# Performance work log

Measured on AMD Instinct MI355X. Metric: run time of the kernel, lower is better.

The kernel has to match this reference:

```python
import jax, jax.numpy as jnp
import numpy as np

HIDDEN = 2048
HEADS = 16
HEAD_DIM = HIDDEN // HEADS
TOP_K = 256
B, N = 1, 2048


def setup_inputs() -> dict:
    key = jax.random.key(0)
    ks = jax.random.split(key, 9)
    s = 0.02
    return {
        "hidden_states": jax.random.normal(ks[0], (B, N, HIDDEN), jnp.float32),
        "Wq": jax.random.normal(ks[1], (HIDDEN, HIDDEN), jnp.float32) * s,
        "bq": jnp.zeros((HIDDEN,), jnp.float32),
        "Wk": jax.random.normal(ks[2], (HIDDEN, HIDDEN), jnp.float32) * s,
        "bk": jnp.zeros((HIDDEN,), jnp.float32),
        "Wv": jax.random.normal(ks[3], (HIDDEN, HIDDEN), jnp.float32) * s,
        "bv": jnp.zeros((HIDDEN,), jnp.float32),
        "Wo": jax.random.normal(ks[4], (HIDDEN, HIDDEN), jnp.float32) * s,
        "bo": jnp.zeros((HIDDEN,), jnp.float32),
    }


def _split_heads(x):
    b, n, _ = x.shape
    return x.reshape(b, n, HEADS, HEAD_DIM).transpose(0, 2, 1, 3)  # b h n d


def reference(hidden_states, Wq, bq, Wk, bk, Wv, bv, Wo, bo):
    scale = 1.0 / jnp.sqrt(jnp.float32(HEAD_DIM))
    q = _split_heads(hidden_states @ Wq + bq)  # [b,h,n,d]
    k = _split_heads(hidden_states @ Wk + bk)
    v = _split_heads(hidden_states @ Wv + bv)

    # Sparse path (kv_seq_length > attention_window): dense QK^T used only to rank keys.
    scores = jnp.einsum("bhnd,bhmd->bhnm", q, k) * scale  # [b,h,n,n]
    importance = scores.mean(axis=2)  # [b,h,n] aggregate over queries
    _, idx = jax.lax.top_k(importance, TOP_K)  # [b,h,k]

    # gather selected K/V (torch.gather along seq dim)
    k_sel = jnp.take_along_axis(k, idx[..., None], axis=2)  # [b,h,k,d]
    v_sel = jnp.take_along_axis(v, idx[..., None], axis=2)

    w = jax.nn.softmax(jnp.einsum("bhnd,bhkd->bhnk", q, k_sel) * scale, axis=-1)
    out = jnp.einsum("bhnk,bhkd->bhnd", w, v_sel)  # [b,h,n,d]
    out = out.transpose(0, 2, 1, 3).reshape(hidden_states.shape[0], -1, HIDDEN)
    return out @ Wo + bo
```

## Files before the change

kernel.cpp:

```cpp
#include <hip/hip_runtime.h>


typedef __attribute__((ext_vector_type(8))) short bf16x8;
typedef __attribute__((ext_vector_type(8))) unsigned short u16x8;
typedef __attribute__((ext_vector_type(4))) float f32x4;

__device__ __forceinline__ unsigned short f2bf(float x) {
    unsigned u = __float_as_uint(x);
    u += 0x7fffu + ((u >> 16) & 1u);
    return (unsigned short)(u >> 16);
}

__device__ __forceinline__ void load_lds16(const unsigned short* g, unsigned short* l) {
    __builtin_amdgcn_global_load_lds(
        (const __attribute__((address_space(1))) unsigned int*)g,
        (__attribute__((address_space(3))) unsigned int*)l,
        16, 0, 0);
}

struct Ptr4  { const float* p[4]; };

__global__ __launch_bounds__(256) void gemm_qkv(
    const unsigned short* __restrict__ HSb,
    const unsigned short* __restrict__ WT4,
    const float* __restrict__ bq,
    const float* __restrict__ bk,
    const float* __restrict__ bv,
    const int* __restrict__ idx,
    unsigned short* __restrict__ Qb,
    unsigned short* __restrict__ Ksel,
    unsigned short* __restrict__ VselT)
{
    __shared__ __align__(16) unsigned short As[4][128][32];
    __shared__ __align__(16) unsigned short Bs[4][64][32];

    const int tid  = threadIdx.x;
    const int lane = tid & 63;
    const int wave = tid >> 6;
    const int wm = wave >> 1, wn = wave & 1;
    const int lr = lane >> 2;
    const int lc = (lane & 3) * 8;

    const int bid = blockIdx.x;

    int kv, h = 0, bm, bn;
    const unsigned short* Bt;
    long ar0, ar1;
    if (bid < 128) {
        kv = 1 + (bid >> 6);
        const int t = bid & 63;
        h  = t >> 2;
        bm = ((t >> 1) & 1) * 128;
        bn = h * 128 + (t & 1) * 64;
        Bt = WT4 + (long)kv * 4194304;
        ar0 = idx[h * 256 + bm + wave * 16 + lr];
        ar1 = idx[h * 256 + bm + wave * 16 + 64 + lr];
    } else {
        kv = 0;
        const int t = bid - 128;
        const int st = t >> 5, u = t & 31;
        bm = ((st >> 2) * 4 + (u >> 3)) * 128;
        bn = ((st & 3) * 8 + (u & 7)) * 64;
        Bt = WT4;
        ar0 = bm + wave * 16 + lr;
        ar1 = ar0 + 64;
    }

    const unsigned short* Arow0 = HSb + ar0 * 2048 + lc;
    const unsigned short* Arow1 = HSb + ar1 * 2048 + lc;
    const unsigned short* Brow0 = Bt + (long)(bn + wave * 16 + lr) * 2048 + lc;

    f32x4 acc[4][2];
#pragma unroll
    for (int i = 0; i < 4; i++)
#pragma unroll
        for (int j = 0; j < 2; j++) acc[i][j] = f32x4{0.f, 0.f, 0.f, 0.f};

    auto stage = [&](int b, int step) {
        const int k0 = step * 32;
        load_lds16(Arow0 + k0, &As[b][wave * 16][0]);
        load_lds16(Arow1 + k0, &As[b][wave * 16 + 64][0]);
        load_lds16(Brow0 + k0, &Bs[b][wave * 16][0]);
    };
    auto compute = [&](int b) {
        bf16x8 af[4], bf[2];
#pragma unroll
        for (int s = 0; s < 4; s++)
            af[s] = *(const bf16x8*)&As[b][wm * 64 + s * 16 + (lane & 15)][(lane >> 4) * 8];
#pragma unroll
        for (int t = 0; t < 2; t++)
            bf[t] = *(const bf16x8*)&Bs[b][wn * 32 + t * 16 + (lane & 15)][(lane >> 4) * 8];
#pragma unroll
        for (int s = 0; s < 4; s++)
#pragma unroll
            for (int t = 0; t < 2; t++)
                acc[s][t] = __builtin_amdgcn_mfma_f32_16x16x32_bf16(af[s], bf[t], acc[s][t], 0, 0, 0);
    };

    stage(0, 0);
    stage(1, 1);
    stage(2, 2);
#pragma unroll 4
    for (int t = 0; t < 61; ++t) {
        asm volatile("s_waitcnt vmcnt(6)" ::: "memory");
        __builtin_amdgcn_s_barrier();
        __builtin_amdgcn_sched_barrier(0);
        stage((t + 3) & 3, t + 3);
        __builtin_amdgcn_sched_barrier(0);
        compute(t & 3);
    }
    asm volatile("s_waitcnt vmcnt(6)" ::: "memory");
    __builtin_amdgcn_s_barrier();
    __builtin_amdgcn_sched_barrier(0);
    compute(1);
    asm volatile("s_waitcnt vmcnt(3)" ::: "memory");
    __builtin_amdgcn_s_barrier();
    __builtin_amdgcn_sched_barrier(0);
    compute(2);
    asm volatile("s_waitcnt vmcnt(0)" ::: "memory");
    __builtin_amdgcn_s_barrier();
    __builtin_amdgcn_sched_barrier(0);
    compute(3);

    if (kv == 0) {
#pragma unroll
        for (int s = 0; s < 4; s++) {
#pragma unroll
            for (int t = 0; t < 2; t++) {
                const int col  = bn + wn * 32 + t * 16 + (lane & 15);
                const int row0 = bm + wm * 64 + s * 16 + (lane >> 4) * 4;
                const float bb = bq[col];
#pragma unroll
                for (int r = 0; r < 4; r++)
                    Qb[(long)(row0 + r) * 2048 + col] = f2bf(acc[s][t][r] + bb);
            }
        }
    } else {
        const float* bp = (kv == 1) ? bk : bv;
#pragma unroll
        for (int s = 0; s < 4; s++) {
#pragma unroll
            for (int t = 0; t < 2; t++) {
                const int col = bn + wn * 32 + t * 16 + (lane & 15);
                const int dd  = col & 127;
                const float bb = bp[col];
                const int j0 = bm + wm * 64 + s * 16 + (lane >> 4) * 4;
#pragma unroll
                for (int r = 0; r < 4; r++) {
                    const int j = j0 + r;
                    const unsigned short h16 = f2bf(acc[s][t][r] + bb);
                    if (kv == 1) Ksel [h * 32768 + j * 128 + dd] = h16;
                    else         VselT[h * 32768 + dd * 256 + j] = h16;
                }
            }
        }
    }
}

__global__ __launch_bounds__(256) void gemm_o(
    const unsigned short* __restrict__ Att,
    const unsigned short* __restrict__ WoT,
    const float* __restrict__ bo,
    float* __restrict__ out)
{
    __shared__ __align__(16) unsigned short As[4][128][32];
    __shared__ __align__(16) unsigned short Bs[4][64][32];

    const int tid  = threadIdx.x;
    const int lane = tid & 63;
    const int wave = tid >> 6;
    const int wm = wave >> 1, wn = wave & 1;
    const int lr  = lane >> 2;
    const int scc = (((lane & 3) ^ ((lr >> 1) & 3))) * 8;
    const int rc  = (((lane >> 4) ^ (((lane & 15) >> 1) & 3))) * 8;

    const int t0 = blockIdx.x;
    const int tl = (t0 & 7) * 64 + (t0 >> 3);
    const int st = tl >> 5, u = tl & 31;
    const int bm = ((st >> 2) * 4 + (u >> 3)) * 128;
    const int bn = ((st & 3) * 8 + (u & 7)) * 64;

    const unsigned short* Arow0 = Att + (long)(bm + wave * 16 + lr) * 2048 + scc;
    const unsigned short* Arow1 = Arow0 + 64 * 2048;
    const unsigned short* Brow0 = WoT + (long)(bn + wave * 16 + lr) * 2048 + scc;

    f32x4 acc[4][2];
#pragma unroll
    for (int i = 0; i < 4; i++)
#pragma unroll
        for (int j = 0; j < 2; j++) acc[i][j] = f32x4{0.f, 0.f, 0.f, 0.f};

    auto stage = [&](int b, int step) {
        const int k0 = step * 32;
        load_lds16(Arow0 + k0, &As[b][wave * 16][0]);
        load_lds16(Arow1 + k0, &As[b][wave * 16 + 64][0]);
        load_lds16(Brow0 + k0, &Bs[b][wave * 16][0]);
    };
    auto compute = [&](int b) {
        bf16x8 af[4], bf[2];
#pragma unroll
        for (int s = 0; s < 4; s++)
            af[s] = *(const bf16x8*)&As[b][wm * 64 + s * 16 + (lane & 15)][rc];
#pragma unroll
        for (int t = 0; t < 2; t++)
            bf[t] = *(const bf16x8*)&Bs[b][wn * 32 + t * 16 + (lane & 15)][rc];
#pragma unroll
        for (int s = 0; s < 4; s++)
#pragma unroll
            for (int t = 0; t < 2; t++)
                acc[s][t] = __builtin_amdgcn_mfma_f32_16x16x32_bf16(af[s], bf[t], acc[s][t], 0, 0, 0);
    };

    stage(0, 0);
    stage(1, 1);
    stage(2, 2);
#pragma unroll 4
    for (int t = 0; t < 61; ++t) {
        asm volatile("s_waitcnt vmcnt(6)" ::: "memory");
        __builtin_amdgcn_s_barrier();
        __builtin_amdgcn_sched_barrier(0);
        stage((t + 3) & 3, t + 3);
        __builtin_amdgcn_sched_barrier(0);
        compute(t & 3);
    }
    asm volatile("s_waitcnt vmcnt(6)" ::: "memory");
    __builtin_amdgcn_s_barrier();
    __builtin_amdgcn_sched_barrier(0);
    compute(1);
    asm volatile("s_waitcnt vmcnt(3)" ::: "memory");
    __builtin_amdgcn_s_barrier();
    __builtin_amdgcn_sched_barrier(0);
    compute(2);
    asm volatile("s_waitcnt vmcnt(0)" ::: "memory");
    __builtin_amdgcn_s_barrier();
    __builtin_amdgcn_sched_barrier(0);
    compute(3);

#pragma unroll
    for (int s = 0; s < 4; s++) {
#pragma unroll
        for (int t = 0; t < 2; t++) {
            const int col  = bn + wn * 32 + t * 16 + (lane & 15);
            const int row0 = bm + wm * 64 + s * 16 + (lane >> 4) * 4;
            const float bb = bo[col];
#pragma unroll
            for (int r = 0; r < 4; r++)
                out[(long)(row0 + r) * 2048 + col] = acc[s][t][r] + bb;
        }
    }
}

#define QS_OFF(c)  ((c) * 2048)
#define KS_OFF(c)  (4096 + (c) * 8192)
#define PS_OFF     0
#define VS_OFF(c)  (16896 + (c) * 4096)

__global__ __launch_bounds__(256, 2) void attn_kernel(
    const unsigned short* __restrict__ Qb,
    const unsigned short* __restrict__ Ksel,
    const unsigned short* __restrict__ VselT,
    unsigned short* __restrict__ Att)
{
    __shared__ __align__(16) unsigned short smem[25088];
    __shared__ float linv[64];

    const int tid  = threadIdx.x;
    const int lane = tid & 63;
    const int wave = tid >> 6;
    const int bm = blockIdx.x * 64;
    const int h  = blockIdx.y;
    const int lr  = lane >> 2;
    const int scc = (((lane & 3) ^ ((lr >> 1) & 3))) * 8;
    const int rc  = (((lane >> 4) ^ (((lane & 15) >> 1) & 3))) * 8;

    const unsigned short* Kh = Ksel  + h * 32768;
    const unsigned short* Vh = VselT + h * 32768;

    f32x4 acc[16];
#pragma unroll
    for (int t = 0; t < 16; t++) acc[t] = f32x4{0.f, 0.f, 0.f, 0.f};

#pragma unroll
    for (int c2 = 0; c2 < 2; c2++) {
        __syncthreads();
#pragma unroll
        for (int c = 0; c < 2; c++) {
            const int k0 = c2 * 64 + c * 32;
            load_lds16(Qb + (long)(bm + wave * 16 + lr) * 2048 + h * 128 + k0 + scc,
                       &smem[QS_OFF(c) + wave * 512]);
#pragma unroll
            for (int q = 0; q < 4; q++)
                load_lds16(Kh + (wave * 64 + q * 16 + lr) * 128 + k0 + scc,
                           &smem[KS_OFF(c) + (wave * 64 + q * 16) * 32]);
        }
        __syncthreads();
#pragma unroll
        for (int kk = 0; kk < 2; kk++) {
            bf16x8 af = *(const bf16x8*)&smem[QS_OFF(kk) + (wave * 16 + (lane & 15)) * 32 + rc];
#pragma unroll
            for (int t = 0; t < 16; t++) {
                bf16x8 bfv = *(const bf16x8*)&smem[KS_OFF(kk) + (t * 16 + (lane & 15)) * 32 + rc];
                acc[t] = __builtin_amdgcn_mfma_f32_16x16x32_bf16(af, bfv, acc[t], 0, 0, 0);
            }
        }
    }
    __syncthreads();

    const float se = 0.08838834764831845f * 1.4426950408889634f;
#pragma unroll
    for (int r = 0; r < 4; r++) {
        float mx = -3.0e38f;
#pragma unroll
        for (int t = 0; t < 16; t++) mx = fmaxf(mx, acc[t][r]);
#pragma unroll
        for (int off = 1; off < 16; off <<= 1) mx = fmaxf(mx, __shfl_xor(mx, off));
        float sum = 0.f;
#pragma unroll
        for (int t = 0; t < 16; t++) {
            float p = exp2f((acc[t][r] - mx) * se);
            acc[t][r] = p;
            sum += p;
        }
#pragma unroll
        for (int off = 1; off < 16; off <<= 1) sum += __shfl_xor(sum, off);
        const int row = wave * 16 + (lane >> 4) * 4 + r;
#pragma unroll
        for (int t = 0; t < 16; t++)
            smem[PS_OFF + row * 264 + t * 16 + (lane & 15)] = f2bf(acc[t][r]);
        if ((lane & 15) == 0) linv[row] = 1.0f / sum;
    }

    const int wm2 = wave >> 1, wn2 = wave & 1;
    f32x4 acc2[2][4];
#pragma unroll
    for (int i = 0; i < 2; i++)
#pragma unroll
        for (int j = 0; j < 4; j++) acc2[i][j] = f32x4{0.f, 0.f, 0.f, 0.f};

#pragma unroll
    for (int c2 = 0; c2 < 4; c2++) {
#pragma unroll
        for (int c = 0; c < 2; c++) {
            const int j0 = c2 * 64 + c * 32;
#pragma unroll
            for (int q = 0; q < 2; q++)
                load_lds16(Vh + (wave * 32 + q * 16 + lr) * 256 + j0 + scc,
                           &smem[VS_OFF(c) + (wave * 32 + q * 16) * 32]);
        }
        __syncthreads();
#pragma unroll
        for (int c = 0; c < 2; c++) {
            const int j0 = c2 * 64 + c * 32;
            bf16x8 af2[2], bf2v[4];
#pragma unroll
            for (int s2 = 0; s2 < 2; s2++)
                af2[s2] = *(const bf16x8*)&smem[PS_OFF + (wm2 * 32 + s2 * 16 + (lane & 15)) * 264 + j0 + (lane >> 4) * 8];
#pragma unroll
            for (int t2 = 0; t2 < 4; t2++)
                bf2v[t2] = *(const bf16x8*)&smem[VS_OFF(c) + (wn2 * 64 + t2 * 16 + (lane & 15)) * 32 + rc];
#pragma unroll
            for (int s2 = 0; s2 < 2; s2++)
#pragma unroll
                for (int t2 = 0; t2 < 4; t2++)
                    acc2[s2][t2] = __builtin_amdgcn_mfma_f32_16x16x32_bf16(af2[s2], bf2v[t2], acc2[s2][t2], 0, 0, 0);
        }
        __syncthreads();
    }

#pragma unroll
    for (int s2 = 0; s2 < 2; s2++) {
#pragma unroll
        for (int t2 = 0; t2 < 4; t2++) {
            const int d = wn2 * 64 + t2 * 16 + (lane & 15);
#pragma unroll
            for (int r = 0; r < 4; r++) {
                const int row = wm2 * 32 + s2 * 16 + (lane >> 4) * 4 + r;
                float v = acc2[s2][t2][r] * linv[row];
                Att[(long)(bm + row) * 2048 + h * 128 + d] = f2bf(v);
            }
        }
    }
}

__global__ __launch_bounds__(256) void prep_kernel(Ptr4 srcs, unsigned short* __restrict__ WT4,
                                                   const float* __restrict__ hs,
                                                   double* __restrict__ part) {
    const int b = blockIdx.x;
    const int tid = threadIdx.x;
    if (b < 4096) {
        __shared__ float tile[64][65];
        const int z = b >> 10, xy = b & 1023;
        const float* W = srcs.p[z];
        unsigned short* WT = WT4 + (long)z * 4194304;
        const int bx = (xy & 31) * 64;
        const int by = (xy >> 5) * 64;
        const int x = tid & 63, y = tid >> 6;
#pragma unroll
        for (int i = 0; i < 64; i += 4)
            tile[y + i][x] = W[(long)(by + y + i) * 2048 + bx + x];
        __syncthreads();
#pragma unroll
        for (int i = 0; i < 64; i += 4)
            WT[(long)(bx + y + i) * 2048 + by + x] = f2bf(tile[x][y + i]);
    } else {
        const int c = b - 4096;
        const int col = (c & 7) * 256 + tid;
        const int r0  = (c >> 3) * 32;
        double a = 0.0;
#pragma unroll 4
        for (int r = 0; r < 32; r++) a += (double)hs[(long)(r0 + r) * 2048 + col];
        part[(long)(c >> 3) * 2048 + col] = a;
    }
}

__global__ void fill_kernel(float* p, float v, long n) {
    long i = ((long)blockIdx.x * blockDim.x + threadIdx.x) * 4;
    if (i + 3 < n) { p[i] = v; p[i+1] = v; p[i+2] = v; p[i+3] = v; }
}

__global__ __launch_bounds__(256) void mean_qsum_part(const double* __restrict__ part,
                                                      const float* __restrict__ Wq,
                                                      double* __restrict__ partq) {
    __shared__ float hsb[32];
    const int j  = blockIdx.x * 256 + threadIdx.x;
    const int i0 = blockIdx.y * 32;
    if (threadIdx.x < 32) {
        double s = 0.0;
#pragma unroll 4
        for (int g = 0; g < 64; g++) s += part[(long)g * 2048 + i0 + threadIdx.x];
        hsb[threadIdx.x] = (float)(s * (1.0 / 2048.0));
    }
    __syncthreads();
    double a = 0.0;
#pragma unroll 4
    for (int r = 0; r < 32; r++)
        a += (double)hsb[r] * (double)Wq[(long)(i0 + r) * 2048 + j];
    partq[(long)blockIdx.y * 2048 + j] = a;
}

__global__ void qsum_fin(const double* __restrict__ partq, const float* __restrict__ bq,
                         float* __restrict__ qbar) {
    const int j = blockIdx.x * 64 + threadIdx.x;
    double s = (double)bq[j];
#pragma unroll 4
    for (int g = 0; g < 64; g++) s += partq[(long)g * 2048 + j];
    qbar[j] = (float)s;
}

__global__ __launch_bounds__(256) void u_kernel(const float* __restrict__ Wk,
                                                const float* __restrict__ qbar,
                                                float* __restrict__ U) {
    const int i = blockIdx.x, t = threadIdx.x;
#pragma unroll
    for (int r = 0; r < 2; r++) {
        const int e = r * 1024 + t * 4;
        float4 w = *(const float4*)(Wk + (long)i * 2048 + e);
        float4 q = *(const float4*)(qbar + e);
        float a = w.x * q.x + w.y * q.y + w.z * q.z + w.w * q.w;
#pragma unroll
        for (int off = 16; off; off >>= 1) a += __shfl_xor(a, off);
        if ((t & 31) == 0) U[(long)i * 16 + r * 8 + (t >> 5)] = a;
    }
}

__global__ __launch_bounds__(256) void cast_imp_kernel(const float* __restrict__ hs,
                                                       const float* __restrict__ U,
                                                       unsigned short* __restrict__ HSb,
                                                       float* __restrict__ imp) {
    __shared__ float red[4][4][16];
    const int m0 = blockIdx.x * 4, t = threadIdx.x;

    float va[4][8];
#pragma unroll
    for (int r = 0; r < 4; r++) {
        const float4 v0 = *(const float4*)(hs + (long)(m0 + r) * 2048 + t * 8);
        const float4 v1 = *(const float4*)(hs + (long)(m0 + r) * 2048 + t * 8 + 4);
        va[r][0] = v0.x; va[r][1] = v0.y; va[r][2] = v0.z; va[r][3] = v0.w;
        va[r][4] = v1.x; va[r][5] = v1.y; va[r][6] = v1.z; va[r][7] = v1.w;
        u16x8 hb;
#pragma unroll
        for (int j = 0; j < 8; j++) hb[j] = f2bf(va[r][j]);
        *(u16x8*)(HSb + (long)(m0 + r) * 2048 + t * 8) = hb;
    }

    float p[4][16];
#pragma unroll
    for (int r = 0; r < 4; r++)
#pragma unroll
        for (int h = 0; h < 16; h++) p[r][h] = 0.f;

    const float4* Uq = (const float4*)(U + (long)t * 128);
#pragma unroll
    for (int j = 0; j < 8; j++) {
        const float4 u0 = Uq[j * 4 + 0];
        const float4 u1 = Uq[j * 4 + 1];
        const float4 u2 = Uq[j * 4 + 2];
        const float4 u3 = Uq[j * 4 + 3];
#pragma unroll
        for (int r = 0; r < 4; r++) {
            const float v = va[r][j];
            p[r][0]  += v * u0.x; p[r][1]  += v * u0.y; p[r][2]  += v * u0.z; p[r][3]  += v * u0.w;
            p[r][4]  += v * u1.x; p[r][5]  += v * u1.y; p[r][6]  += v * u1.z; p[r][7]  += v * u1.w;
            p[r][8]  += v * u2.x; p[r][9]  += v * u2.y; p[r][10] += v * u2.z; p[r][11] += v * u2.w;
            p[r][12] += v * u3.x; p[r][13] += v * u3.y; p[r][14] += v * u3.z; p[r][15] += v * u3.w;
        }
    }

#pragma unroll
    for (int off = 32; off; off >>= 1)
#pragma unroll
        for (int r = 0; r < 4; r++)
#pragma unroll
            for (int h = 0; h < 16; h++) p[r][h] += __shfl_down(p[r][h], off);
    if ((t & 63) == 0)
#pragma unroll
        for (int r = 0; r < 4; r++)
#pragma unroll
            for (int h = 0; h < 16; h++) red[t >> 6][r][h] = p[r][h];
    __syncthreads();
    if (t < 64) {
        const int h = t & 15, r = t >> 4;
        imp[(long)h * 2048 + m0 + r] =
            red[0][r][h] + red[1][r][h] + red[2][r][h] + red[3][r][h];
    }
}

__global__ __launch_bounds__(64) void topk_idx(const float* __restrict__ imp,
                                               int* __restrict__ idx) {
    const int h = blockIdx.x;
    const int lane = threadIdx.x;
    unsigned u[32];
#pragma unroll
    for (int r = 0; r < 32; r++) {
        unsigned x = __float_as_uint(imp[(long)h * 2048 + r * 64 + lane]);
        u[r] = (x & 0x80000000u) ? ~x : (x | 0x80000000u);
    }
    unsigned cur = 0;
    for (int b = 31; b >= 0; b--) {
        const unsigned cand = cur | (1u << b);
        int tot = 0;
#pragma unroll
        for (int r = 0; r < 32; r++)
            tot += (int)__popcll(__ballot(u[r] >= cand));
        if (tot >= 256) cur = cand;
    }
    const unsigned long long below = (1ull << lane) - 1ull;
    int pos[32];
    int base = 0;
#pragma unroll
    for (int r = 0; r < 32; r++) {
        const bool q = u[r] > cur;
        const unsigned long long m = __ballot(q);
        pos[r] = q ? base + (int)__popcll(m & below) : -1;
        base += (int)__popcll(m);
    }
#pragma unroll
    for (int r = 0; r < 32; r++) {
        const bool q = (u[r] == cur);
        const unsigned long long m = __ballot(q);
        if (q) {
            const int p = base + (int)__popcll(m & below);
            pos[r] = (p < 256) ? p : -1;
        }
        base += (int)__popcll(m);
    }
#pragma unroll
    for (int r = 0; r < 32; r++)
        if (pos[r] >= 0) idx[h * 256 + pos[r]] = r * 64 + lane;
}

extern "C" void kernel_launch(void* const* d_in, const int* in_sizes, int n_in,
                              void* d_out, int out_size, void* d_ws, size_t ws_size,
                              hipStream_t stream)
{
    const float* hs = (const float*)d_in[0];
    const float* Wq = (const float*)d_in[1];
    const float* bq = (const float*)d_in[2];
    const float* Wk = (const float*)d_in[3];
    const float* bk = (const float*)d_in[4];
    const float* Wv = (const float*)d_in[5];
    const float* bv = (const float*)d_in[6];
    const float* Wo = (const float*)d_in[7];
    const float* bo = (const float*)d_in[8];

    char* ws = (char*)d_ws;
    size_t off = 0;
    auto alloc = [&](size_t b) -> void* {
        void* p = ws + off;
        off = (off + b + 255) & ~(size_t)255;
        return p;
    };
    unsigned short* HSb   = (unsigned short*)alloc(8388608);
    unsigned short* WT4   = (unsigned short*)alloc(4 * 8388608);
    unsigned short* Qb    = (unsigned short*)alloc(8388608);
    unsigned short* Att   = (unsigned short*)alloc(8388608);
    unsigned short* Ksel  = (unsigned short*)alloc(1048576);
    unsigned short* VselT = (unsigned short*)alloc(1048576);
    double* part  = (double*)alloc(1048576);
    double* partq = (double*)alloc(1048576);
    float* qbar  = (float*)alloc(8192);
    float* U     = (float*)alloc(131072);
    float* imp   = (float*)alloc(131072);
    int*   idx   = (int*)alloc(16384);

    if (off > ws_size) {
        fill_kernel<<<4096, 256, 0, stream>>>((float*)d_out, 12345.0f, (long)out_size);
        return;
    }

    unsigned short* WoT = WT4 + 3 * 4194304;

    prep_kernel<<<4608, 256, 0, stream>>>(Ptr4{{Wq, Wk, Wv, Wo}}, WT4, hs, part);

    mean_qsum_part<<<dim3(8, 64), 256, 0, stream>>>(part, Wq, partq);
    qsum_fin<<<32, 64, 0, stream>>>(partq, bq, qbar);
    u_kernel<<<2048, 256, 0, stream>>>(Wk, qbar, U);
    cast_imp_kernel<<<512, 256, 0, stream>>>(hs, U, HSb, imp);

    topk_idx<<<16, 64, 0, stream>>>(imp, idx);

    gemm_qkv<<<640, 256, 0, stream>>>(HSb, WT4, bq, bk, bv, idx, Qb, Ksel, VselT);

    attn_kernel<<<dim3(32, 16), 256, 0, stream>>>(Qb, Ksel, VselT, Att);

    gemm_o<<<512, 256, 0, stream>>>(Att, WoT, bo, (float*)d_out);
}
```

Baseline: 278.1 us.

## Fuse Q projection into attention kernel and split off K/V selection GEMM

The Q projection is moved out of the combined QKV GEMM and into the attention kernel. Each attention block now computes its 64x128 Q tile from hidden states and Wq straight into LDS, which removes the Qb round trip through global memory. The QKV launch shrinks to a 128-block K/V-only kernel, so the attention launch is now serialized behind a smaller GEMM. In exchange, attention LDS use grows, which may reduce occupancy, and the per-block Q GEMM uses a smaller tile with less reuse of hidden-state rows than the previous 128x64 tiling.

```diff
diff --git a/kernel.cpp b/kernel.cpp
--- a/kernel.cpp
+++ b/kernel.cpp
@@ -20,14 +20,12 @@
 
 struct Ptr4  { const float* p[4]; };
 
-__global__ __launch_bounds__(256) void gemm_qkv(
+__global__ __launch_bounds__(256) void gemm_kv(
     const unsigned short* __restrict__ HSb,
     const unsigned short* __restrict__ WT4,
-    const float* __restrict__ bq,
     const float* __restrict__ bk,
     const float* __restrict__ bv,
     const int* __restrict__ idx,
-    unsigned short* __restrict__ Qb,
     unsigned short* __restrict__ Ksel,
     unsigned short* __restrict__ VselT)
 {
@@ -42,29 +40,14 @@
     const int lc = (lane & 3) * 8;
 
     const int bid = blockIdx.x;
-
-    int kv, h = 0, bm, bn;
-    const unsigned short* Bt;
-    long ar0, ar1;
-    if (bid < 128) {
-        kv = 1 + (bid >> 6);
-        const int t = bid & 63;
-        h  = t >> 2;
-        bm = ((t >> 1) & 1) * 128;
-        bn = h * 128 + (t & 1) * 64;
-        Bt = WT4 + (long)kv * 4194304;
-        ar0 = idx[h * 256 + bm + wave * 16 + lr];
-        ar1 = idx[h * 256 + bm + wave * 16 + 64 + lr];
-    } else {
-        kv = 0;
-        const int t = bid - 128;
-        const int st = t >> 5, u = t & 31;
-        bm = ((st >> 2) * 4 + (u >> 3)) * 128;
-        bn = ((st & 3) * 8 + (u & 7)) * 64;
-        Bt = WT4;
-        ar0 = bm + wave * 16 + lr;
-        ar1 = ar0 + 64;
-    }
+    const int kv = 1 + (bid >> 6);
+    const int t = bid & 63;
+    const int h  = t >> 2;
+    const int bm = ((t >> 1) & 1) * 128;
+    const int bn = h * 128 + (t & 1) * 64;
+    const unsigned short* Bt = WT4 + (long)kv * 4194304;
+    const long ar0 = idx[h * 256 + bm + wave * 16 + lr];
+    const long ar1 = idx[h * 256 + bm + wave * 16 + 64 + lr];
 
     const unsigned short* Arow0 = HSb + ar0 * 2048 + lc;
     const unsigned short* Arow1 = HSb + ar1 * 2048 + lc;
@@ -88,26 +71,26 @@
         for (int s = 0; s < 4; s++)
             af[s] = *(const bf16x8*)&As[b][wm * 64 + s * 16 + (lane & 15)][(lane >> 4) * 8];
 #pragma unroll
-        for (int t = 0; t < 2; t++)
-            bf[t] = *(const bf16x8*)&Bs[b][wn * 32 + t * 16 + (lane & 15)][(lane >> 4) * 8];
+        for (int t2 = 0; t2 < 2; t2++)
+            bf[t2] = *(const bf16x8*)&Bs[b][wn * 32 + t2 * 16 + (lane & 15)][(lane >> 4) * 8];
 #pragma unroll
         for (int s = 0; s < 4; s++)
 #pragma unroll
-            for (int t = 0; t < 2; t++)
-                acc[s][t] = __builtin_amdgcn_mfma_f32_16x16x32_bf16(af[s], bf[t], acc[s][t], 0, 0, 0);
+            for (int t2 = 0; t2 < 2; t2++)
+                acc[s][t2] = __builtin_amdgcn_mfma_f32_16x16x32_bf16(af[s], bf[t2], acc[s][t2], 0, 0, 0);
     };
 
     stage(0, 0);
     stage(1, 1);
     stage(2, 2);
 #pragma unroll 4
-    for (int t = 0; t < 61; ++t) {
+    for (int t2 = 0; t2 < 61; ++t2) {
         asm volatile("s_waitcnt vmcnt(6)" ::: "memory");
         __builtin_amdgcn_s_barrier();
         __builtin_amdgcn_sched_barrier(0);
-        stage((t + 3) & 3, t + 3);
+        stage((t2 + 3) & 3, t2 + 3);
         __builtin_amdgcn_sched_barrier(0);
-        compute(t & 3);
+        compute(t2 & 3);
     }
     asm volatile("s_waitcnt vmcnt(6)" ::: "memory");
     __builtin_amdgcn_s_barrier();
@@ -122,36 +105,21 @@
     __builtin_amdgcn_sched_barrier(0);
     compute(3);
 
-    if (kv == 0) {
-#pragma unroll
-        for (int s = 0; s < 4; s++) {
-#pragma unroll
-            for (int t = 0; t < 2; t++) {
-                const int col  = bn + wn * 32 + t * 16 + (lane & 15);
-                const int row0 = bm + wm * 64 + s * 16 + (lane >> 4) * 4;
-                const float bb = bq[col];
-#pragma unroll
-                for (int r = 0; r < 4; r++)
-                    Qb[(long)(row0 + r) * 2048 + col] = f2bf(acc[s][t][r] + bb);
-            }
-        }
-    } else {
-        const float* bp = (kv == 1) ? bk : bv;
-#pragma unroll
-        for (int s = 0; s < 4; s++) {
-#pragma unroll
-            for (int t = 0; t < 2; t++) {
-                const int col = bn + wn * 32 + t * 16 + (lane & 15);
-                const int dd  = col & 127;
-                const float bb = bp[col];
-                const int j0 = bm + wm * 64 + s * 16 + (lane >> 4) * 4;
-#pragma unroll
-                for (int r = 0; r < 4; r++) {
-                    const int j = j0 + r;
-                    const unsigned short h16 = f2bf(acc[s][t][r] + bb);
-                    if (kv == 1) Ksel [h * 32768 + j * 128 + dd] = h16;
-                    else         VselT[h * 32768 + dd * 256 + j] = h16;
-                }
+    const float* bp = (kv == 1) ? bk : bv;
+#pragma unroll
+    for (int s = 0; s < 4; s++) {
+#pragma unroll
+        for (int t2 = 0; t2 < 2; t2++) {
+            const int col = bn + wn * 32 + t2 * 16 + (lane & 15);
+            const int dd  = col & 127;
+            const float bb = bp[col];
+            const int j0 = bm + wm * 64 + s * 16 + (lane >> 4) * 4;
+#pragma unroll
+            for (int r = 0; r < 4; r++) {
+                const int j = j0 + r;
+                const unsigned short h16 = f2bf(acc[s][t2][r] + bb);
+                if (kv == 1) Ksel [h * 32768 + j * 128 + dd] = h16;
+                else         VselT[h * 32768 + dd * 256 + j] = h16;
             }
         }
     }
@@ -250,18 +218,20 @@
     }
 }
 
-#define QS_OFF(c)  ((c) * 2048)
-#define KS_OFF(c)  (4096 + (c) * 8192)
-#define PS_OFF     0
-#define VS_OFF(c)  (16896 + (c) * 4096)
-
-__global__ __launch_bounds__(256, 2) void attn_kernel(
-    const unsigned short* __restrict__ Qb,
+#define KS2_OFF(c)  ((c) * 8192)
+#define PS2_OFF     0
+#define QS2_OFF     24576
+#define VS2_OFF(c)  (24576 + (c) * 4096)
+
+__global__ __launch_bounds__(256, 2) void attn_fused(
+    const unsigned short* __restrict__ HSb,
+    const unsigned short* __restrict__ WT4,
+    const float* __restrict__ bq,
     const unsigned short* __restrict__ Ksel,
     const unsigned short* __restrict__ VselT,
     unsigned short* __restrict__ Att)
 {
-    __shared__ __align__(16) unsigned short smem[25088];
+    __shared__ __align__(16) unsigned short smem[33280];
     __shared__ float linv[64];
 
     const int tid  = threadIdx.x;
@@ -270,12 +240,88 @@
     const int bm = blockIdx.x * 64;
     const int h  = blockIdx.y;
     const int lr  = lane >> 2;
+    const int lc  = (lane & 3) * 8;
     const int scc = (((lane & 3) ^ ((lr >> 1) & 3))) * 8;
     const int rc  = (((lane >> 4) ^ (((lane & 15) >> 1) & 3))) * 8;
 
     const unsigned short* Kh = Ksel  + h * 32768;
     const unsigned short* Vh = VselT + h * 32768;
 
+    {
+        const unsigned short* Arow = HSb + (long)(bm + wave * 16 + lr) * 2048 + lc;
+        const unsigned short* Brow0 = WT4 + (long)(h * 128 + wave * 16 + lr) * 2048 + lc;
+        const unsigned short* Brow1 = Brow0 + 64 * 2048;
+
+        f32x4 acc[4][2];
+#pragma unroll
+        for (int i = 0; i < 4; i++)
+#pragma unroll
+            for (int j = 0; j < 2; j++) acc[i][j] = f32x4{0.f, 0.f, 0.f, 0.f};
+
+        auto stage = [&](int b, int step) {
+            const int k0 = step * 32;
+            load_lds16(Arow + k0, &smem[b * 2048 + wave * 16 * 32]);
+            load_lds16(Brow0 + k0, &smem[8192 + b * 4096 + wave * 16 * 32]);
+            load_lds16(Brow1 + k0, &smem[8192 + b * 4096 + (64 + wave * 16) * 32]);
+        };
+        auto compute = [&](int b) {
+            bf16x8 af[4], bf[2];
+#pragma unroll
+            for (int s = 0; s < 4; s++)
+                af[s] = *(const bf16x8*)&smem[b * 2048 + (s * 16 + (lane & 15)) * 32 + (lane >> 4) * 8];
+#pragma unroll
+            for (int t = 0; t < 2; t++)
+                bf[t] = *(const bf16x8*)&smem[8192 + b * 4096 + (wave * 32 + t * 16 + (lane & 15)) * 32 + (lane >> 4) * 8];
+#pragma unroll
+            for (int s = 0; s < 4; s++)
+#pragma unroll
+                for (int t = 0; t < 2; t++)
+                    acc[s][t] = __builtin_amdgcn_mfma_f32_16x16x32_bf16(af[s], bf[t], acc[s][t], 0, 0, 0);
+        };
+
+        stage(0, 0);
+        stage(1, 1);
+        stage(2, 2);
+#pragma unroll 4
+        for (int t = 0; t < 61; ++t) {
+            asm volatile("s_waitcnt vmcnt(6)" ::: "memory");
+            __builtin_amdgcn_s_barrier();
+            __builtin_amdgcn_sched_barrier(0);
+            stage((t + 3) & 3, t + 3);
+            __builtin_amdgcn_sched_barrier(0);
+            compute(t & 3);
+        }
+        asm volatile("s_waitcnt vmcnt(6)" ::: "memory");
+        __builtin_amdgcn_s_barrier();
+        __builtin_amdgcn_sched_barrier(0);
+        compute(1);
+        asm volatile("s_waitcnt vmcnt(3)" ::: "memory");
+        __builtin_amdgcn_s_barrier();
+        __builtin_amdgcn_sched_barrier(0);
+        compute(2);
+        asm volatile("s_waitcnt vmcnt(0)" ::: "memory");
+        __builtin_amdgcn_s_barrier();
+        __builtin_amdgcn_sched_barrier(0);
+        compute(3);
+
+        float bb[2];
+#pragma unroll
+        for (int t = 0; t < 2; t++)
+            bb[t] = bq[h * 128 + wave * 32 + t * 16 + (lane & 15)];
+#pragma unroll
+        for (int s = 0; s < 4; s++)
+#pragma unroll
+            for (int t = 0; t < 2; t++) {
+                const int col = wave * 32 + t * 16 + (lane & 15);
+#pragma unroll
+                for (int r = 0; r < 4; r++) {
+                    const int row = s * 16 + (lane >> 4) * 4 + r;
+                    smem[QS2_OFF + row * 136 + col] = f2bf(acc[s][t][r] + bb[t]);
+                }
+            }
+    }
+    __syncthreads();
+
     f32x4 acc[16];
 #pragma unroll
     for (int t = 0; t < 16; t++) acc[t] = f32x4{0.f, 0.f, 0.f, 0.f};
@@ -286,20 +332,19 @@
 #pragma unroll
         for (int c = 0; c < 2; c++) {
             const int k0 = c2 * 64 + c * 32;
-            load_lds16(Qb + (long)(bm + wave * 16 + lr) * 2048 + h * 128 + k0 + scc,
-                       &smem[QS_OFF(c) + wave * 512]);
 #pragma unroll
             for (int q = 0; q < 4; q++)
                 load_lds16(Kh + (wave * 64 + q * 16 + lr) * 128 + k0 + scc,
-                           &smem[KS_OFF(c) + (wave * 64 + q * 16) * 32]);
+                           &smem[KS2_OFF(c) + (wave * 64 + q * 16) * 32]);
         }
         __syncthreads();
 #pragma unroll
         for (int kk = 0; kk < 2; kk++) {
-            bf16x8 af = *(const bf16x8*)&smem[QS_OFF(kk) + (wave * 16 + (lane & 15)) * 32 + rc];
+            bf16x8 af = *(const bf16x8*)&smem[QS2_OFF + (wave * 16 + (lane & 15)) * 136
+                                              + c2 * 64 + kk * 32 + (lane >> 4) * 8];
 #pragma unroll
             for (int t = 0; t < 16; t++) {
-                bf16x8 bfv = *(const bf16x8*)&smem[KS_OFF(kk) + (t * 16 + (lane & 15)) * 32 + rc];
+                bf16x8 bfv = *(const bf16x8*)&smem[KS2_OFF(kk) + (t * 16 + (lane & 15)) * 32 + rc];
                 acc[t] = __builtin_amdgcn_mfma_f32_16x16x32_bf16(af, bfv, acc[t], 0, 0, 0);
             }
         }
@@ -326,7 +371,7 @@
         const int row = wave * 16 + (lane >> 4) * 4 + r;
 #pragma unroll
         for (int t = 0; t < 16; t++)
-            smem[PS_OFF + row * 264 + t * 16 + (lane & 15)] = f2bf(acc[t][r]);
+            smem[PS2_OFF + row * 264 + t * 16 + (lane & 15)] = f2bf(acc[t][r]);
         if ((lane & 15) == 0) linv[row] = 1.0f / sum;
     }
 
@@ -345,7 +390,7 @@
 #pragma unroll
             for (int q = 0; q < 2; q++)
                 load_lds16(Vh + (wave * 32 + q * 16 + lr) * 256 + j0 + scc,
-                           &smem[VS_OFF(c) + (wave * 32 + q * 16) * 32]);
+                           &smem[VS2_OFF(c) + (wave * 32 + q * 16) * 32]);
         }
         __syncthreads();
 #pragma unroll
@@ -354,10 +399,10 @@
             bf16x8 af2[2], bf2v[4];
 #pragma unroll
             for (int s2 = 0; s2 < 2; s2++)
-                af2[s2] = *(const bf16x8*)&smem[PS_OFF + (wm2 * 32 + s2 * 16 + (lane & 15)) * 264 + j0 + (lane >> 4) * 8];
+                af2[s2] = *(const bf16x8*)&smem[PS2_OFF + (wm2 * 32 + s2 * 16 + (lane & 15)) * 264 + j0 + (lane >> 4) * 8];
 #pragma unroll
             for (int t2 = 0; t2 < 4; t2++)
-                bf2v[t2] = *(const bf16x8*)&smem[VS_OFF(c) + (wn2 * 64 + t2 * 16 + (lane & 15)) * 32 + rc];
+                bf2v[t2] = *(const bf16x8*)&smem[VS2_OFF(c) + (wn2 * 64 + t2 * 16 + (lane & 15)) * 32 + rc];
 #pragma unroll
             for (int s2 = 0; s2 < 2; s2++)
 #pragma unroll
@@ -592,7 +637,6 @@
     };
     unsigned short* HSb   = (unsigned short*)alloc(8388608);
     unsigned short* WT4   = (unsigned short*)alloc(4 * 8388608);
-    unsigned short* Qb    = (unsigned short*)alloc(8388608);
     unsigned short* Att   = (unsigned short*)alloc(8388608);
     unsigned short* Ksel  = (unsigned short*)alloc(1048576);
     unsigned short* VselT = (unsigned short*)alloc(1048576);
@@ -619,9 +663,9 @@
 
     topk_idx<<<16, 64, 0, stream>>>(imp, idx);
 
-    gemm_qkv<<<640, 256, 0, stream>>>(HSb, WT4, bq, bk, bv, idx, Qb, Ksel, VselT);
-
-    attn_kernel<<<dim3(32, 16), 256, 0, stream>>>(Qb, Ksel, VselT, Att);
+    gemm_kv<<<128, 256, 0, stream>>>(HSb, WT4, bk, bv, idx, Ksel, VselT);
+
+    attn_fused<<<dim3(32, 16), 256, 0, stream>>>(HSb, WT4, bq, Ksel, VselT, Att);
 
     gemm_o<<<512, 256, 0, stream>>>(Att, WoT, bo, (float*)d_out);
 }
```

After: 293.0 us. 1.05x slower.

## Load QKV GEMM B operand directly to registers and drop block barriers

Applied to the files above, without the earlier changes.

The QKV projection GEMM now gives each wave its own 32-row A slice, staged in a private LDS region. Each wave loads the full 64-column B tile straight from global memory into registers, double-buffered. This removes shared B staging and all workgroup barriers from the main loop, since waves no longer share LDS data. The cost is that every wave re-reads the same B data from global/L2, four times the B traffic, plus more VGPR pressure from register double buffering. The vmcnt waits now have to cover both the direct loads and the LDS DMA.

```diff
diff --git a/kernel.cpp b/kernel.cpp
--- a/kernel.cpp
+++ b/kernel.cpp
@@ -31,13 +31,11 @@
     unsigned short* __restrict__ Ksel,
     unsigned short* __restrict__ VselT)
 {
-    __shared__ __align__(16) unsigned short As[4][128][32];
-    __shared__ __align__(16) unsigned short Bs[4][64][32];
+    __shared__ __align__(16) unsigned short As[4][4][32][32];
 
     const int tid  = threadIdx.x;
     const int lane = tid & 63;
     const int wave = tid >> 6;
-    const int wm = wave >> 1, wn = wave & 1;
     const int lr = lane >> 2;
     const int lc = (lane & 3) * 8;
 
@@ -53,8 +51,8 @@
         bm = ((t >> 1) & 1) * 128;
         bn = h * 128 + (t & 1) * 64;
         Bt = WT4 + (long)kv * 4194304;
-        ar0 = idx[h * 256 + bm + wave * 16 + lr];
-        ar1 = idx[h * 256 + bm + wave * 16 + 64 + lr];
+        ar0 = idx[h * 256 + bm + wave * 32 + lr];
+        ar1 = idx[h * 256 + bm + wave * 32 + 16 + lr];
     } else {
         kv = 0;
         const int t = bid - 128;
@@ -62,93 +60,107 @@
         bm = ((st >> 2) * 4 + (u >> 3)) * 128;
         bn = ((st & 3) * 8 + (u & 7)) * 64;
         Bt = WT4;
-        ar0 = bm + wave * 16 + lr;
-        ar1 = ar0 + 64;
+        ar0 = bm + wave * 32 + lr;
+        ar1 = ar0 + 16;
     }
 
     const unsigned short* Arow0 = HSb + ar0 * 2048 + lc;
     const unsigned short* Arow1 = HSb + ar1 * 2048 + lc;
-    const unsigned short* Brow0 = Bt + (long)(bn + wave * 16 + lr) * 2048 + lc;
-
-    f32x4 acc[4][2];
-#pragma unroll
-    for (int i = 0; i < 4; i++)
-#pragma unroll
-        for (int j = 0; j < 2; j++) acc[i][j] = f32x4{0.f, 0.f, 0.f, 0.f};
-
-    auto stage = [&](int b, int step) {
+    const unsigned short* Bl = Bt + (long)(bn + (lane & 15)) * 2048 + (lane >> 4) * 8;
+
+    unsigned short* ldsw = &As[0][wave][0][0];
+
+    f32x4 acc[2][4];
+#pragma unroll
+    for (int i = 0; i < 2; i++)
+#pragma unroll
+        for (int j = 0; j < 4; j++) acc[i][j] = f32x4{0.f, 0.f, 0.f, 0.f};
+
+    bf16x8 b0[4], b1[4];
+
+    auto loadB = [&](bf16x8* b, int step) {
         const int k0 = step * 32;
-        load_lds16(Arow0 + k0, &As[b][wave * 16][0]);
-        load_lds16(Arow1 + k0, &As[b][wave * 16 + 64][0]);
-        load_lds16(Brow0 + k0, &Bs[b][wave * 16][0]);
+#pragma unroll
+        for (int tt = 0; tt < 4; tt++)
+            b[tt] = *(const bf16x8*)(Bl + (long)tt * 32768 + k0);
     };
-    auto compute = [&](int b) {
-        bf16x8 af[4], bf[2];
-#pragma unroll
-        for (int s = 0; s < 4; s++)
-            af[s] = *(const bf16x8*)&As[b][wm * 64 + s * 16 + (lane & 15)][(lane >> 4) * 8];
-#pragma unroll
-        for (int t = 0; t < 2; t++)
-            bf[t] = *(const bf16x8*)&Bs[b][wn * 32 + t * 16 + (lane & 15)][(lane >> 4) * 8];
-#pragma unroll
-        for (int s = 0; s < 4; s++)
-#pragma unroll
-            for (int t = 0; t < 2; t++)
-                acc[s][t] = __builtin_amdgcn_mfma_f32_16x16x32_bf16(af[s], bf[t], acc[s][t], 0, 0, 0);
+    auto stageA = [&](int buf, int step) {
+        const int k0 = step * 32;
+        load_lds16(Arow0 + k0, ldsw + buf * 4096);
+        load_lds16(Arow1 + k0, ldsw + buf * 4096 + 512);
     };
-
-    stage(0, 0);
-    stage(1, 1);
-    stage(2, 2);
-#pragma unroll 4
-    for (int t = 0; t < 61; ++t) {
+    auto compute = [&](int buf, const bf16x8* b) {
+        bf16x8 af[2];
+#pragma unroll
+        for (int s = 0; s < 2; s++)
+            af[s] = *(const bf16x8*)(ldsw + buf * 4096 + (s * 16 + (lane & 15)) * 32 + (lane >> 4) * 8);
+#pragma unroll
+        for (int s = 0; s < 2; s++)
+#pragma unroll
+            for (int tt = 0; tt < 4; tt++)
+                acc[s][tt] = __builtin_amdgcn_mfma_f32_16x16x32_bf16(af[s], b[tt], acc[s][tt], 0, 0, 0);
+    };
+
+    stageA(0, 0);
+    stageA(1, 1);
+    __builtin_amdgcn_sched_barrier(0);
+    loadB(b0, 0);
+    __builtin_amdgcn_sched_barrier(0);
+
+    for (int t2 = 0; t2 < 31; ++t2) {
+        const int te = 2 * t2;
+        loadB(b1, te + 1);
+        __builtin_amdgcn_sched_barrier(0);
+        stageA((te + 2) & 3, te + 2);
+        __builtin_amdgcn_sched_barrier(0);
         asm volatile("s_waitcnt vmcnt(6)" ::: "memory");
-        __builtin_amdgcn_s_barrier();
-        __builtin_amdgcn_sched_barrier(0);
-        stage((t + 3) & 3, t + 3);
-        __builtin_amdgcn_sched_barrier(0);
-        compute(t & 3);
-    }
+        __builtin_amdgcn_sched_barrier(0);
+        compute(te & 3, b0);
+
+        loadB(b0, te + 2);
+        __builtin_amdgcn_sched_barrier(0);
+        stageA((te + 3) & 3, te + 3);
+        __builtin_amdgcn_sched_barrier(0);
+        asm volatile("s_waitcnt vmcnt(6)" ::: "memory");
+        __builtin_amdgcn_sched_barrier(0);
+        compute((te + 1) & 3, b1);
+    }
+    loadB(b1, 63);
+    __builtin_amdgcn_sched_barrier(0);
     asm volatile("s_waitcnt vmcnt(6)" ::: "memory");
-    __builtin_amdgcn_s_barrier();
-    __builtin_amdgcn_sched_barrier(0);
-    compute(1);
-    asm volatile("s_waitcnt vmcnt(3)" ::: "memory");
-    __builtin_amdgcn_s_barrier();
-    __builtin_amdgcn_sched_barrier(0);
-    compute(2);
+    __builtin_amdgcn_sched_barrier(0);
+    compute(62 & 3, b0);
     asm volatile("s_waitcnt vmcnt(0)" ::: "memory");
-    __builtin_amdgcn_s_barrier();
-    __builtin_amdgcn_sched_barrier(0);
-    compute(3);
+    __builtin_amdgcn_sched_barrier(0);
+    compute(63 & 3, b1);
 
     if (kv == 0) {
 #pragma unroll
-        for (int s = 0; s < 4; s++) {
-#pragma unroll
-            for (int t = 0; t < 2; t++) {
-                const int col  = bn + wn * 32 + t * 16 + (lane & 15);
-                const int row0 = bm + wm * 64 + s * 16 + (lane >> 4) * 4;
+        for (int s = 0; s < 2; s++) {
+#pragma unroll
+            for (int tt = 0; tt < 4; tt++) {
+                const int col  = bn + tt * 16 + (lane & 15);
+                const int row0 = bm + wave * 32 + s * 16 + (lane >> 4) * 4;
                 const float bb = bq[col];
 #pragma unroll
                 for (int r = 0; r < 4; r++)
-                    Qb[(long)(row0 + r) * 2048 + col] = f2bf(acc[s][t][r] + bb);
+                    Qb[(long)(row0 + r) * 2048 + col] = f2bf(acc[s][tt][r] + bb);
             }
         }
     } else {
         const float* bp = (kv == 1) ? bk : bv;
 #pragma unroll
-        for (int s = 0; s < 4; s++) {
-#pragma unroll
-            for (int t = 0; t < 2; t++) {
-                const int col = bn + wn * 32 + t * 16 + (lane & 15);
+        for (int s = 0; s < 2; s++) {
+#pragma unroll
+            for (int tt = 0; tt < 4; tt++) {
+                const int col = bn + tt * 16 + (lane & 15);
                 const int dd  = col & 127;
                 const float bb = bp[col];
-                const int j0 = bm + wm * 64 + s * 16 + (lane >> 4) * 4;
+                const int j0 = bm + wave * 32 + s * 16 + (lane >> 4) * 4;
 #pragma unroll
                 for (int r = 0; r < 4; r++) {
                     const int j = j0 + r;
-                    const unsigned short h16 = f2bf(acc[s][t][r] + bb);
+                    const unsigned short h16 = f2bf(acc[s][tt][r] + bb);
                     if (kv == 1) Ksel [h * 32768 + j * 128 + dd] = h16;
                     else         VselT[h * 32768 + dd * 256 + j] = h16;
                 }
```

Result: slower. 346.0 us (+24.4%).
